# Kernel optimization log

Measured on AMD Instinct MI355X. Metric: run time of the kernel, lower is better.

The kernel has to match this reference:

```python
import jax, jax.numpy as jnp
import numpy as np
import math

H = 16  # heads
EPS = 1e-5

def _gelu_tanh(x):
    c = math.sqrt(2.0 / math.pi)
    return 0.5 * x * (1.0 + jnp.tanh(c * (x + 0.044715 * x * x * x)))

def _layernorm(x, g, b):
    mu = jnp.mean(x, axis=-1, keepdims=True)
    var = jnp.mean((x - mu) ** 2, axis=-1, keepdims=True)
    return (x - mu) / jnp.sqrt(var + EPS) * g + b


def setup_inputs() -> dict:
    key = jax.random.key(0)
    ks = jax.random.split(key, 16)
    B, S, D, F = 8, 1024, 1024, 4096
    s = 1.0 / math.sqrt(D)
    inp = {
        "x": jax.random.normal(ks[0], (B, S, D), jnp.float32),
        "mask": jax.random.randint(ks[1], (B, 1, S, S), 0, 2, jnp.int32),
        "Wq": jax.random.normal(ks[2], (D, D), jnp.float32) * s,
        "bq": jnp.zeros((D,), jnp.float32),
        "Wk": jax.random.normal(ks[3], (D, D), jnp.float32) * s,
        "bk": jnp.zeros((D,), jnp.float32),
        "Wv": jax.random.normal(ks[4], (D, D), jnp.float32) * s,
        "bv": jnp.zeros((D,), jnp.float32),
        "Wo": jax.random.normal(ks[5], (D, D), jnp.float32) * s,
        "bo": jnp.zeros((D,), jnp.float32),
        "W1": jax.random.normal(ks[6], (D, F), jnp.float32) * s,
        "b1": jnp.zeros((F,), jnp.float32),
        "W2": jax.random.normal(ks[7], (F, D), jnp.float32) * (1.0 / math.sqrt(F)),
        "b2": jnp.zeros((D,), jnp.float32),
        "ln1_g": jnp.ones((D,), jnp.float32),
        "ln1_b": jnp.zeros((D,), jnp.float32),
        "ln2_g": jnp.ones((D,), jnp.float32),
        "ln2_b": jnp.zeros((D,), jnp.float32),
    }
    return inp


def reference(x, mask, Wq, bq, Wk, bk, Wv, bv, Wo, bo, W1, b1, W2, b2,
              ln1_g, ln1_b, ln2_g, ln2_b):
    B, S, D = x.shape
    dk = D // H

    # --- sublayer 1: pre-LN multi-head attention + residual ---
    y = _layernorm(x, ln1_g, ln1_b)
    q = (y @ Wq + bq).reshape(B, S, H, dk).transpose(0, 2, 1, 3)  # [B,H,S,dk]
    k = (y @ Wk + bk).reshape(B, S, H, dk).transpose(0, 2, 1, 3)
    v = (y @ Wv + bv).reshape(B, S, H, dk).transpose(0, 2, 1, 3)

    scores = jnp.einsum('bhqd,bhkd->bhqk', q, k) / jnp.sqrt(jnp.float32(dk))
    scores = jnp.where(mask == 0, jnp.float32(-1e9), scores)
    p = jax.nn.softmax(scores, axis=-1)
    a = jnp.einsum('bhqk,bhkd->bhqd', p, v)
    a = a.transpose(0, 2, 1, 3).reshape(B, S, D)
    x = x + (a @ Wo + bo)

    # --- sublayer 2: pre-LN GELU FFN + residual ---
    y = _layernorm(x, ln2_g, ln2_b)
    h = _gelu_tanh(y @ W1 + b1)
    return x + (h @ W2 + b2)
```

## Files before the change

kernel.cpp:

```cpp
#include <hip/hip_runtime.h>
#include <math.h>

typedef unsigned short u16;
typedef short bf16x8 __attribute__((ext_vector_type(8)));
typedef float f32x4 __attribute__((ext_vector_type(4)));

#define DEV static __device__ __forceinline__

DEV float bf2f(u16 u) {
  union { unsigned int i; float f; } v; v.i = ((unsigned int)u) << 16; return v.f;
}
DEV u16 f2bf(float f) {
  union { float f; unsigned int i; } v; v.f = f;
  unsigned int x = v.i;
  return (u16)((x + 0x7FFFu + ((x >> 16) & 1u)) >> 16);
}

DEV void gload16(const void* gsrc, void* ldst) {
  __builtin_amdgcn_global_load_lds(
      (__attribute__((address_space(1))) void*)gsrc,
      (__attribute__((address_space(3))) void*)ldst, 16, 0, 0);
}

DEV f32x4 mfma16(bf16x8 a, bf16x8 b, f32x4 c) {
  return __builtin_amdgcn_mfma_f32_16x16x32_bf16(a, b, c, 0, 0, 0);
}

template <int EPI, int WF32, int NFR>
__global__ __launch_bounds__(512, 2)
void gemm8(const u16* __restrict__ A, const u16* __restrict__ Bt,
           const float* __restrict__ bias, const float* __restrict__ res,
           void* __restrict__ Cv, int M, int N, int K) {
  constexpr int BN = NFR * 64;
  constexpr int HB = NFR * 4096;
  __shared__ __align__(16) char Alds[4 * 16384];
  __shared__ __align__(16) char Blds[4 * HB];

  const int ntn = N / BN;
  const int nwg = gridDim.x;
  const int cpx = nwg >> 3;
  const int bid = (int)blockIdx.x;
  const int swb = (bid & 7) * cpx + (bid >> 3);
  const int tm = swb / ntn, tn = swb % ntn;

  const int tid = threadIdx.x;
  const int wave = tid >> 6, lane = tid & 63;
  const int wm = wave >> 2, wn = wave & 3;
  const int lg = lane >> 4, lr = lane & 15;
  const int swx = (lr & 7) << 4;

  f32x4 acc[8][NFR];
#pragma unroll
  for (int m = 0; m < 8; ++m)
#pragma unroll
    for (int n = 0; n < NFR; ++n)
#pragma unroll
      for (int r = 0; r < 4; ++r) acc[m][n][r] = 0.f;

  const size_t rowb = (size_t)K * 2;
  const char* Ab = (const char*)A + (size_t)tm * 256 * rowb;
  const char* Bb = (const char*)Bt + (size_t)tn * BN * rowb;

  int rowS[2], colS[2];
#pragma unroll
  for (int rr = 0; rr < 2; ++rr) {
    const int p = rr * 8192 + tid * 16;
    const int f = p ^ (((p >> 7) & 7) << 4);
    rowS[rr] = f >> 7; colS[rr] = f & 127;
  }

  const int NT = K >> 6;

#define SA(T, H)                                                              \
  do {                                                                        \
    char* d_ = Alds + ((((T) & 1) * 2 + (H)) << 14);                          \
    _Pragma("unroll")                                                         \
    for (int r_ = 0; r_ < 2; ++r_)                                            \
      gload16(Ab + (size_t)((H) * 128 + rowS[r_]) * rowb + (size_t)(T) * 128  \
                  + colS[r_],                                                 \
              d_ + r_ * 8192 + wave * 1024);                                  \
  } while (0)

#define SB(T, H)                                                              \
  do {                                                                        \
    char* d_ = Blds + ((((T) & 1) * 2 + (H)) * HB);                           \
    _Pragma("unroll")                                                         \
    for (int r_ = 0; r_ < NFR / 2; ++r_)                                      \
      gload16(Bb + (size_t)((H) * (BN / 2) + rowS[r_]) * rowb                 \
                  + (size_t)(T) * 128 + colS[r_],                             \
              d_ + r_ * 8192 + wave * 1024);                                  \
  } while (0)

#define PHASE(SS, Q, STG, DOVM)                                               \
  {                                                                           \
    if ((Q) == 0) {                                                           \
      _Pragma("unroll")                                                       \
      for (int n_ = 0; n_ < NFR; ++n_) {                                      \
        const int g_ = n_ * 4 + wn;                                           \
        const char* bs_ = Blds + ((SS) * 2 + g_ / (NFR * 2)) * HB;            \
        const int rb_ = (g_ % (NFR * 2)) * 16 + lr;                           \
        _Pragma("unroll")                                                     \
        for (int k_ = 0; k_ < 2; ++k_)                                        \
          bfr[n_][k_] =                                                       \
              *(const bf16x8*)(bs_ + ((rb_ * 128 + k_ * 64 + lg * 16) ^ swx));\
      }                                                                       \
    }                                                                         \
    bf16x8 af_[2][2];                                                         \
    {                                                                         \
      const char* as_ = Alds + (((SS) * 2 + ((Q) >> 1)) << 14);               \
      _Pragma("unroll")                                                       \
      for (int j_ = 0; j_ < 2; ++j_) {                                        \
        const int ra_ = ((4 * (Q) + 2 * j_ + wm) & 7) * 16 + lr;              \
        _Pragma("unroll")                                                     \
        for (int k_ = 0; k_ < 2; ++k_)                                        \
          af_[j_][k_] =                                                       \
              *(const bf16x8*)(as_ + ((ra_ * 128 + k_ * 64 + lg * 16) ^ swx));\
      }                                                                       \
    }                                                                         \
    STG;                                                                      \
    if ((Q) == 0) asm volatile("s_waitcnt lgkmcnt(8)");                       \
    if ((DOVM) == 1) {                                                        \
      if (NFR == 4) asm volatile("s_waitcnt vmcnt(6)");                       \
      else          asm volatile("s_waitcnt vmcnt(4)");                       \
    } else if ((DOVM) == 2) {                                                 \
      asm volatile("s_waitcnt vmcnt(0)");                                     \
    }                                                                         \
    __builtin_amdgcn_s_barrier();                                             \
    asm volatile("s_waitcnt lgkmcnt(0)");                                     \
    __builtin_amdgcn_sched_barrier(0);                                        \
    __builtin_amdgcn_s_setprio(1);                                            \
    _Pragma("unroll")                                                         \
    for (int j_ = 0; j_ < 2; ++j_)                                            \
      _Pragma("unroll")                                                       \
      for (int n_ = 0; n_ < NFR; ++n_)                                        \
        _Pragma("unroll")                                                     \
        for (int k_ = 0; k_ < 2; ++k_)                                        \
          acc[2 * (Q) + j_][n_] =                                             \
              mfma16(af_[j_][k_], bfr[n_][k_], acc[2 * (Q) + j_][n_]);        \
    __builtin_amdgcn_s_setprio(0);                                            \
    __builtin_amdgcn_s_barrier();                                             \
  }

  SA(0, 0); SA(0, 1); SB(0, 0); SB(0, 1); SA(1, 0); SB(1, 0); SB(1, 1);
  asm volatile("s_waitcnt vmcnt(0)");
  __builtin_amdgcn_s_barrier();

  bf16x8 bfr[NFR][2];
  const int NIT = NT >> 1;
  for (int it = 0; it < NIT - 1; ++it) {
    const int T0 = 2 * it;
    PHASE(0, 0, SA(T0 + 1, 1), 0)
    PHASE(0, 1, SB(T0 + 2, 0), 0)
    PHASE(0, 2, SA(T0 + 2, 0), 0)
    PHASE(0, 3, SB(T0 + 2, 1), 1)
    PHASE(1, 0, SA(T0 + 2, 1), 0)
    PHASE(1, 1, SB(T0 + 3, 0), 0)
    PHASE(1, 2, SB(T0 + 3, 1), 0)
    PHASE(1, 3, SA(T0 + 3, 0), 1)
  }
  {
    const int T0 = NT - 2;
    PHASE(0, 0, SA(T0 + 1, 1), 0)
    PHASE(0, 1, ((void)0), 0)
    PHASE(0, 2, ((void)0), 0)
    PHASE(0, 3, ((void)0), 2)
    PHASE(1, 0, ((void)0), 0)
    PHASE(1, 1, ((void)0), 0)
    PHASE(1, 2, ((void)0), 0)
    PHASE(1, 3, ((void)0), 0)
  }
#undef SA
#undef SB
#undef PHASE

#pragma unroll
  for (int m = 0; m < 8; ++m)
#pragma unroll
    for (int n = 0; n < NFR; ++n) {
      const int col = tn * BN + (n * 4 + wn) * 16 + lr;
      const float bc = bias[col];
#pragma unroll
      for (int r = 0; r < 4; ++r) {
        const int row = tm * 256 + (2 * m + wm) * 16 + lg * 4 + r;
        float vv = acc[m][n][r] + bc;
        if (EPI == 1) {
          const float u = vv;
          const float z = u + 0.044715f * u * u * u;
          vv = u * __builtin_amdgcn_rcpf(1.0f + exp2f(-2.3022076954f * z));
        } else if (EPI == 2) {
          vv += res[(size_t)row * N + col];
        } else if (EPI == 3) {
          vv *= 0.180336880111112f;
        }
        if (WF32)
          ((float*)Cv)[(size_t)row * N + col] = vv;
        else
          ((u16*)Cv)[(size_t)row * N + col] = f2bf(vv);
      }
    }
}

__global__ __launch_bounds__(256)
void attn_kernel(const u16* __restrict__ Q, const u16* __restrict__ Km,
                 const u16* __restrict__ Vt, const u16* __restrict__ maskT4,
                 u16* __restrict__ O) {
  const int bid = (int)blockIdx.x;
  const int swz = (bid & 7) * 256 + (bid >> 3);
  const int qb = swz & 15;
  const int bh = swz >> 4;
  const int b = bh >> 4, h = bh & 15;
  const int wave = threadIdx.x >> 6, lane = threadIdx.x & 63;
  const int lg = lane >> 4, lr = lane & 15;
  __shared__ __align__(16) u16 Ksm[2][64 * 64];
  __shared__ __align__(16) u16 Vsm[2][64 * 64];
  __shared__ __align__(16) u16 Pl[4][1024];
  char* Pb = (char*)&Pl[wave][0];
  const int swx = (lr & 7) << 4;

  const int q0 = qb * 64 + wave * 16;
  const u16* Qp = Q + ((size_t)(b * 1024 + q0)) * 1024 + h * 64;
  bf16x8 qf[2];
#pragma unroll
  for (int ks = 0; ks < 2; ++ks)
    qf[ks] = *(const bf16x8*)(Qp + (size_t)lr * 1024 + ks * 32 + lg * 8);

  float l = 0.f;
  f32x4 accO[4];
#pragma unroll
  for (int fc = 0; fc < 4; ++fc)
#pragma unroll
    for (int r = 0; r < 4; ++r) accO[fc][r] = 0.f;

  const char* Kg = (const char*)(Km + (size_t)(b * 1024) * 1024 + h * 64);
  const char* Vg = (const char*)(Vt + (size_t)(bh * 64) * 1024);
  const ushort4* Mb0 = (const ushort4*)maskT4 + (size_t)b * 256 * 1024 + q0 + lr;

#define STAGE_KV(T, BUF)                                                      \
  {                                                                           \
    const int kb_ = (T) * 64;                                                 \
    _Pragma("unroll")                                                         \
    for (int c = 0; c < 2; ++c) {                                             \
      const int chunk = wave * 2 + c;                                         \
      const int p = chunk * 1024 + lane * 16;                                 \
      const int f = p ^ (((p >> 7) & 7) << 4);                                \
      const int row = f >> 7, colb = f & 127;                                 \
      gload16(Kg + (size_t)(kb_ + row) * 2048 + colb,                         \
              (char*)Ksm[BUF] + chunk * 1024);                                \
      gload16(Vg + (size_t)row * 2048 + (size_t)kb_ * 2 + colb,               \
              (char*)Vsm[BUF] + chunk * 1024);                                \
    }                                                                         \
  }

  STAGE_KV(0, 0);
  __syncthreads();

  for (int t = 0; t < 16; ++t) {
    const int cb = t & 1;
    if (t < 15) STAGE_KV(t + 1, cb ^ 1);

    ushort4 mv[4];
#pragma unroll
    for (int fc = 0; fc < 4; ++fc)
      mv[fc] = Mb0[(size_t)(t * 16 + fc * 4 + lg) * 1024];

    f32x4 ts[4];
#pragma unroll
    for (int fc = 0; fc < 4; ++fc)
#pragma unroll
      for (int r = 0; r < 4; ++r) ts[fc][r] = 0.f;
    __builtin_amdgcn_s_setprio(1);
#pragma unroll
    for (int ks = 0; ks < 2; ++ks)
#pragma unroll
      for (int fc = 0; fc < 4; ++fc) {
        const int row = fc * 16 + lr;
        const int ad = ((row << 7) | (ks * 64 + lg * 16)) ^ ((row & 7) << 4);
        const bf16x8 kfr = *(const bf16x8*)((const char*)Ksm[cb] + ad);
        ts[fc] = mfma16(kfr, qf[ks], ts[fc]);
      }
    __builtin_amdgcn_s_setprio(0);

#pragma unroll
    for (int fc = 0; fc < 4; ++fc) {
      const float p0 = exp2f(ts[fc][0] + bf2f(mv[fc].x));
      const float p1 = exp2f(ts[fc][1] + bf2f(mv[fc].y));
      const float p2 = exp2f(ts[fc][2] + bf2f(mv[fc].z));
      const float p3 = exp2f(ts[fc][3] + bf2f(mv[fc].w));
      l += (p0 + p1) + (p2 + p3);
      unsigned int w0, w1;
      asm("v_cvt_pk_bf16_f32 %0, %1, %2" : "=v"(w0) : "v"(p0), "v"(p1));
      asm("v_cvt_pk_bf16_f32 %0, %1, %2" : "=v"(w1) : "v"(p2), "v"(p3));
      const int base = lr * 128 + fc * 32 + lg * 8;
      *(unsigned int*)(Pb + ((base + 0) ^ swx)) = w0;
      *(unsigned int*)(Pb + ((base + 4) ^ swx)) = w1;
    }

    __builtin_amdgcn_s_setprio(1);
#pragma unroll
    for (int ks = 0; ks < 2; ++ks) {
      const int ad = (lr * 128 + ks * 64 + lg * 16) ^ swx;
      const bf16x8 pa = *(const bf16x8*)(Pb + ad);
#pragma unroll
      for (int fc = 0; fc < 4; ++fc) {
        const int row = fc * 16 + lr;
        const int vad = ((row << 7) | (ks * 64 + lg * 16)) ^ ((row & 7) << 4);
        const bf16x8 vfr = *(const bf16x8*)((const char*)Vsm[cb] + vad);
        accO[fc] = mfma16(pa, vfr, accO[fc]);
      }
    }
    __builtin_amdgcn_s_setprio(0);

    __syncthreads();
  }

  l += __shfl_xor(l, 16);
  l += __shfl_xor(l, 32);
  float linv[4];
#pragma unroll
  for (int r = 0; r < 4; ++r) linv[r] = 1.0f / __shfl(l, lg * 4 + r);

  u16* Op = O + ((size_t)(b * 1024 + q0)) * 1024 + h * 64;
#pragma unroll
  for (int fc = 0; fc < 4; ++fc)
#pragma unroll
    for (int r = 0; r < 4; ++r)
      Op[(size_t)(lg * 4 + r) * 1024 + fc * 16 + lr] = f2bf(accO[fc][r] * linv[r]);
#undef STAGE_KV
}

__global__ __launch_bounds__(256)
void transpose_cast(const float* __restrict__ in, u16* __restrict__ out, int R, int C) {
  __shared__ u16 t[64][65];
  const int ctiles = C >> 6;
  const int bx = blockIdx.x % ctiles, by = blockIdx.x / ctiles;
  const int tc = threadIdx.x & 63, t4 = threadIdx.x >> 6;
#pragma unroll
  for (int i = 0; i < 16; ++i) {
    const int r = i * 4 + t4;
    t[r][tc] = f2bf(in[(size_t)(by * 64 + r) * C + bx * 64 + tc]);
  }
  __syncthreads();
#pragma unroll
  for (int i = 0; i < 16; ++i) {
    const int r = i * 4 + t4;
    out[(size_t)(bx * 64 + r) * R + by * 64 + tc] = t[tc][r];
  }
}

__global__ __launch_bounds__(256)
void transpose_v_kernel(const u16* __restrict__ v, u16* __restrict__ vt) {
  const int st = blockIdx.x & 15, bh = blockIdx.x >> 4;
  __shared__ u16 t[64][65];
  const int tc = threadIdx.x & 63, t4 = threadIdx.x >> 6;
  const u16* src = v + ((size_t)((bh >> 4) * 1024 + st * 64)) * 1024 + (bh & 15) * 64;
#pragma unroll
  for (int i = 0; i < 16; ++i) {
    const int r = i * 4 + t4;
    t[r][tc] = src[(size_t)r * 1024 + tc];
  }
  __syncthreads();
  u16* dst = vt + (size_t)bh * 64 * 1024 + st * 64;
#pragma unroll
  for (int i = 0; i < 16; ++i) {
    const int r = i * 4 + t4;
    dst[(size_t)r * 1024 + tc] = t[tc][r];
  }
}

__global__ __launch_bounds__(256)
void mask_t_kernel(const int* __restrict__ mask, u16* __restrict__ mt) {
  const int bt = blockIdx.x;
  const int b = bt >> 8;
  const int kt = (bt >> 4) & 15;
  const int qt = bt & 15;
  __shared__ u16 t[64][65];
  const int tc = threadIdx.x & 63, t4 = threadIdx.x >> 6;
  const u16 neg = f2bf(-1.442695040888963e9f);
  const int* src = mask + ((size_t)b * 1024 + qt * 64) * 1024 + kt * 64;
#pragma unroll
  for (int i = 0; i < 16; ++i) {
    const int q = i * 4 + t4;
    t[q][tc] = src[(size_t)q * 1024 + tc] ? (u16)0 : neg;
  }
  __syncthreads();
  ushort4* dst = (ushort4*)mt + ((size_t)b * 256 + kt * 16) * 1024 + qt * 64;
#pragma unroll
  for (int i = 0; i < 4; ++i) {
    const int kg = i * 4 + t4;
    ushort4 o;
    o.x = t[tc][kg * 4 + 0];
    o.y = t[tc][kg * 4 + 1];
    o.z = t[tc][kg * 4 + 2];
    o.w = t[tc][kg * 4 + 3];
    dst[(size_t)kg * 1024 + tc] = o;
  }
}

__global__ __launch_bounds__(256)
void ln_kernel(const float* __restrict__ x, const float* __restrict__ g,
               const float* __restrict__ bb, u16* __restrict__ y) {
  const int row = blockIdx.x, tid = threadIdx.x;
  const float4 v = ((const float4*)(x + (size_t)row * 1024))[tid];
  float s = v.x + v.y + v.z + v.w;
  float ss = v.x * v.x + v.y * v.y + v.z * v.z + v.w * v.w;
#pragma unroll
  for (int mk = 1; mk < 64; mk <<= 1) {
    s += __shfl_xor(s, mk);
    ss += __shfl_xor(ss, mk);
  }
  __shared__ float sa[4], sq[4];
  const int wave = tid >> 6, lane = tid & 63;
  if (lane == 0) { sa[wave] = s; sq[wave] = ss; }
  __syncthreads();
  s = sa[0] + sa[1] + sa[2] + sa[3];
  ss = sq[0] + sq[1] + sq[2] + sq[3];
  const float mu = s * 0.0009765625f;
  const float var = ss * 0.0009765625f - mu * mu;
  const float inv = rsqrtf(var + 1e-5f);
  const float4 gg = ((const float4*)g)[tid];
  const float4 bv = ((const float4*)bb)[tid];
  ushort4 o;
  o.x = f2bf((v.x - mu) * inv * gg.x + bv.x);
  o.y = f2bf((v.y - mu) * inv * gg.y + bv.y);
  o.z = f2bf((v.z - mu) * inv * gg.z + bv.z);
  o.w = f2bf((v.w - mu) * inv * gg.w + bv.w);
  *(ushort4*)(y + (size_t)row * 1024 + tid * 4) = o;
}

extern "C" void kernel_launch(void* const* d_in, const int* in_sizes, int n_in,
                              void* d_out, int out_size, void* d_ws, size_t ws_size,
                              hipStream_t stream) {
  (void)in_sizes; (void)n_in; (void)out_size; (void)ws_size;
  const float* x  = (const float*)d_in[0];
  const int* mask = (const int*)d_in[1];
  const float* Wq = (const float*)d_in[2];  const float* bq = (const float*)d_in[3];
  const float* Wk = (const float*)d_in[4];  const float* bk = (const float*)d_in[5];
  const float* Wv = (const float*)d_in[6];  const float* bv = (const float*)d_in[7];
  const float* Wo = (const float*)d_in[8];  const float* bo = (const float*)d_in[9];
  const float* W1 = (const float*)d_in[10]; const float* b1 = (const float*)d_in[11];
  const float* W2 = (const float*)d_in[12]; const float* b2 = (const float*)d_in[13];
  const float* g1 = (const float*)d_in[14]; const float* be1 = (const float*)d_in[15];
  const float* g2 = (const float*)d_in[16]; const float* be2 = (const float*)d_in[17];

  float* out = (float*)d_out;

  u16* ws = (u16*)d_ws;
  const size_t M1 = (size_t)1024 * 1024;
  u16* y    = ws;
  u16* q    = ws + 8 * M1;
  u16* kbuf = ws + 16 * M1;
  u16* vbuf = ws + 24 * M1;
  u16* vt   = ws + 32 * M1;
  u16* hbuf = ws + 8 * M1;
  u16* wqt  = ws + 40 * M1;
  u16* wkt  = ws + 41 * M1;
  u16* wvt  = ws + 42 * M1;
  u16* wot  = ws + 43 * M1;
  u16* w1t  = ws + 44 * M1;
  u16* w2t  = ws + 48 * M1;
  u16* maskT4 = y;

  dim3 blk(256);
  dim3 blk8(512);
  transpose_cast<<<256, blk, 0, stream>>>(Wq, wqt, 1024, 1024);
  transpose_cast<<<256, blk, 0, stream>>>(Wk, wkt, 1024, 1024);
  transpose_cast<<<256, blk, 0, stream>>>(Wv, wvt, 1024, 1024);
  transpose_cast<<<256, blk, 0, stream>>>(Wo, wot, 1024, 1024);
  transpose_cast<<<1024, blk, 0, stream>>>(W1, w1t, 1024, 4096);
  transpose_cast<<<1024, blk, 0, stream>>>(W2, w2t, 4096, 1024);
  ln_kernel<<<8192, blk, 0, stream>>>(x, g1, be1, y);
  gemm8<3, 0, 2><<<256, blk8, 0, stream>>>(y, wqt, bq, nullptr, q, 8192, 1024, 1024);
  gemm8<0, 0, 2><<<256, blk8, 0, stream>>>(y, wkt, bk, nullptr, kbuf, 8192, 1024, 1024);
  gemm8<0, 0, 2><<<256, blk8, 0, stream>>>(y, wvt, bv, nullptr, vbuf, 8192, 1024, 1024);
  transpose_v_kernel<<<2048, blk, 0, stream>>>(vbuf, vt);
  mask_t_kernel<<<2048, blk, 0, stream>>>(mask, maskT4);
  attn_kernel<<<2048, blk, 0, stream>>>(q, kbuf, vt, maskT4, vbuf);
  gemm8<2, 1, 2><<<256, blk8, 0, stream>>>(vbuf, wot, bo, x, out, 8192, 1024, 1024);
  ln_kernel<<<8192, blk, 0, stream>>>(out, g2, be2, y);
  gemm8<1, 0, 4><<<512, blk8, 0, stream>>>(y, w1t, b1, nullptr, hbuf, 8192, 4096, 1024);
  gemm8<2, 1, 2><<<256, blk8, 0, stream>>>(hbuf, w2t, b2, out, out, 8192, 1024, 4096);
}
```

Before: 404.5 us.

## Double-buffer LDS fragment reads across phases and fix GEMM tile width

```diff
diff --git a/kernel.cpp b/kernel.cpp
--- a/kernel.cpp
+++ b/kernel.cpp
@@ -26,17 +26,15 @@
   return __builtin_amdgcn_mfma_f32_16x16x32_bf16(a, b, c, 0, 0, 0);
 }
 
-template <int EPI, int WF32, int NFR>
+template <int EPI, int WF32>
 __global__ __launch_bounds__(512, 2)
 void gemm8(const u16* __restrict__ A, const u16* __restrict__ Bt,
            const float* __restrict__ bias, const float* __restrict__ res,
            void* __restrict__ Cv, int M, int N, int K) {
-  constexpr int BN = NFR * 64;
-  constexpr int HB = NFR * 4096;
   __shared__ __align__(16) char Alds[4 * 16384];
-  __shared__ __align__(16) char Blds[4 * HB];
-
-  const int ntn = N / BN;
+  __shared__ __align__(16) char Blds[4 * 8192];
+
+  const int ntn = N >> 7;
   const int nwg = gridDim.x;
   const int cpx = nwg >> 3;
   const int bid = (int)blockIdx.x;
@@ -49,17 +47,17 @@
   const int lg = lane >> 4, lr = lane & 15;
   const int swx = (lr & 7) << 4;
 
-  f32x4 acc[8][NFR];
+  f32x4 acc[8][2];
 #pragma unroll
   for (int m = 0; m < 8; ++m)
 #pragma unroll
-    for (int n = 0; n < NFR; ++n)
+    for (int n = 0; n < 2; ++n)
 #pragma unroll
       for (int r = 0; r < 4; ++r) acc[m][n][r] = 0.f;
 
   const size_t rowb = (size_t)K * 2;
   const char* Ab = (const char*)A + (size_t)tm * 256 * rowb;
-  const char* Bb = (const char*)Bt + (size_t)tn * BN * rowb;
+  const char* Bb = (const char*)Bt + (size_t)tn * 128 * rowb;
 
   int rowS[2], colS[2];
 #pragma unroll
@@ -83,101 +81,112 @@
 
 #define SB(T, H)                                                              \
   do {                                                                        \
-    char* d_ = Blds + ((((T) & 1) * 2 + (H)) * HB);                           \
-    _Pragma("unroll")                                                         \
-    for (int r_ = 0; r_ < NFR / 2; ++r_)                                      \
-      gload16(Bb + (size_t)((H) * (BN / 2) + rowS[r_]) * rowb                 \
-                  + (size_t)(T) * 128 + colS[r_],                             \
-              d_ + r_ * 8192 + wave * 1024);                                  \
+    char* d_ = Blds + ((((T) & 1) * 2 + (H)) * 8192);                         \
+    gload16(Bb + (size_t)((H) * 64 + rowS[0]) * rowb + (size_t)(T) * 128      \
+                + colS[0],                                                    \
+            d_ + wave * 1024);                                                \
   } while (0)
 
-#define PHASE(SS, Q, STG, DOVM)                                               \
+#define RDA(BUF, NSS, NQ)                                                     \
   {                                                                           \
-    if ((Q) == 0) {                                                           \
+    const char* as_ = Alds + (((NSS) * 2 + ((NQ) >> 1)) << 14);               \
+    _Pragma("unroll")                                                         \
+    for (int j_ = 0; j_ < 2; ++j_) {                                          \
+      const int ra_ = ((4 * (NQ) + 2 * j_ + wm) & 7) * 16 + lr;               \
       _Pragma("unroll")                                                       \
-      for (int n_ = 0; n_ < NFR; ++n_) {                                      \
-        const int g_ = n_ * 4 + wn;                                           \
-        const char* bs_ = Blds + ((SS) * 2 + g_ / (NFR * 2)) * HB;            \
-        const int rb_ = (g_ % (NFR * 2)) * 16 + lr;                           \
-        _Pragma("unroll")                                                     \
-        for (int k_ = 0; k_ < 2; ++k_)                                        \
-          bfr[n_][k_] =                                                       \
-              *(const bf16x8*)(bs_ + ((rb_ * 128 + k_ * 64 + lg * 16) ^ swx));\
-      }                                                                       \
+      for (int k_ = 0; k_ < 2; ++k_)                                          \
+        afr[BUF][j_][k_] =                                                    \
+            *(const bf16x8*)(as_ + ((ra_ * 128 + k_ * 64 + lg * 16) ^ swx));  \
     }                                                                         \
-    bf16x8 af_[2][2];                                                         \
-    {                                                                         \
-      const char* as_ = Alds + (((SS) * 2 + ((Q) >> 1)) << 14);               \
+  }
+
+#define RDB(BUF, NSS)                                                         \
+  {                                                                           \
+    _Pragma("unroll")                                                         \
+    for (int n_ = 0; n_ < 2; ++n_) {                                          \
+      const char* bs_ = Blds + ((NSS) * 2 + n_) * 8192;                       \
+      const int rb_ = wn * 16 + lr;                                           \
       _Pragma("unroll")                                                       \
-      for (int j_ = 0; j_ < 2; ++j_) {                                        \
-        const int ra_ = ((4 * (Q) + 2 * j_ + wm) & 7) * 16 + lr;              \
-        _Pragma("unroll")                                                     \
-        for (int k_ = 0; k_ < 2; ++k_)                                        \
-          af_[j_][k_] =                                                       \
-              *(const bf16x8*)(as_ + ((ra_ * 128 + k_ * 64 + lg * 16) ^ swx));\
-      }                                                                       \
+      for (int k_ = 0; k_ < 2; ++k_)                                          \
+        bfr[BUF][n_][k_] =                                                    \
+            *(const bf16x8*)(bs_ + ((rb_ * 128 + k_ * 64 + lg * 16) ^ swx));  \
     }                                                                         \
+  }
+
+#define PHASE(CUR, BB, Q, STG, DOVM, DON, NSS, NQ, DOB)                       \
+  {                                                                           \
     STG;                                                                      \
-    if ((Q) == 0) asm volatile("s_waitcnt lgkmcnt(8)");                       \
-    if ((DOVM) == 1) {                                                        \
-      if (NFR == 4) asm volatile("s_waitcnt vmcnt(6)");                       \
-      else          asm volatile("s_waitcnt vmcnt(4)");                       \
-    } else if ((DOVM) == 2) {                                                 \
-      asm volatile("s_waitcnt vmcnt(0)");                                     \
-    }                                                                         \
+    if ((DOVM) == 1) asm volatile("s_waitcnt vmcnt(4)");                      \
+    else if ((DOVM) == 2) asm volatile("s_waitcnt vmcnt(0)");                 \
     __builtin_amdgcn_s_barrier();                                             \
     asm volatile("s_waitcnt lgkmcnt(0)");                                     \
     __builtin_amdgcn_sched_barrier(0);                                        \
     __builtin_amdgcn_s_setprio(1);                                            \
     _Pragma("unroll")                                                         \
-    for (int j_ = 0; j_ < 2; ++j_)                                            \
+    for (int n_ = 0; n_ < 2; ++n_)                                            \
       _Pragma("unroll")                                                       \
-      for (int n_ = 0; n_ < NFR; ++n_)                                        \
-        _Pragma("unroll")                                                     \
-        for (int k_ = 0; k_ < 2; ++k_)                                        \
-          acc[2 * (Q) + j_][n_] =                                             \
-              mfma16(af_[j_][k_], bfr[n_][k_], acc[2 * (Q) + j_][n_]);        \
+      for (int k_ = 0; k_ < 2; ++k_)                                          \
+        acc[2 * (Q) + 0][n_] =                                                \
+            mfma16(afr[CUR][0][k_], bfr[BB][n_][k_], acc[2 * (Q) + 0][n_]);   \
+    __builtin_amdgcn_sched_barrier(0);                                        \
+    if (DON) {                                                                \
+      RDA((CUR) ^ 1, NSS, NQ);                                                \
+      if (DOB) RDB((BB) ^ 1, NSS);                                            \
+    }                                                                         \
+    __builtin_amdgcn_sched_barrier(0);                                        \
+    _Pragma("unroll")                                                         \
+    for (int n_ = 0; n_ < 2; ++n_)                                            \
+      _Pragma("unroll")                                                       \
+      for (int k_ = 0; k_ < 2; ++k_)                                          \
+        acc[2 * (Q) + 1][n_] =                                                \
+            mfma16(afr[CUR][1][k_], bfr[BB][n_][k_], acc[2 * (Q) + 1][n_]);   \
     __builtin_amdgcn_s_setprio(0);                                            \
     __builtin_amdgcn_s_barrier();                                             \
   }
+
+  bf16x8 afr[2][2][2];
+  bf16x8 bfr[2][2][2];
 
   SA(0, 0); SA(0, 1); SB(0, 0); SB(0, 1); SA(1, 0); SB(1, 0); SB(1, 1);
   asm volatile("s_waitcnt vmcnt(0)");
   __builtin_amdgcn_s_barrier();
-
-  bf16x8 bfr[NFR][2];
+  RDA(0, 0, 0);
+  RDB(0, 0);
+
   const int NIT = NT >> 1;
   for (int it = 0; it < NIT - 1; ++it) {
     const int T0 = 2 * it;
-    PHASE(0, 0, SA(T0 + 1, 1), 0)
-    PHASE(0, 1, SB(T0 + 2, 0), 0)
-    PHASE(0, 2, SA(T0 + 2, 0), 0)
-    PHASE(0, 3, SB(T0 + 2, 1), 1)
-    PHASE(1, 0, SA(T0 + 2, 1), 0)
-    PHASE(1, 1, SB(T0 + 3, 0), 0)
-    PHASE(1, 2, SB(T0 + 3, 1), 0)
-    PHASE(1, 3, SA(T0 + 3, 0), 1)
+    PHASE(0, 0, 0, SA(T0 + 1, 1), 0, 1, 0, 1, 0)
+    PHASE(1, 0, 1, SB(T0 + 2, 0), 0, 1, 0, 2, 0)
+    PHASE(0, 0, 2, SA(T0 + 2, 0), 0, 1, 0, 3, 0)
+    PHASE(1, 0, 3, SB(T0 + 2, 1), 1, 1, 1, 0, 1)
+    PHASE(0, 1, 0, SA(T0 + 2, 1), 0, 1, 1, 1, 0)
+    PHASE(1, 1, 1, SB(T0 + 3, 0), 0, 1, 1, 2, 0)
+    PHASE(0, 1, 2, SB(T0 + 3, 1), 0, 1, 1, 3, 0)
+    PHASE(1, 1, 3, SA(T0 + 3, 0), 1, 1, 0, 0, 1)
   }
   {
     const int T0 = NT - 2;
-    PHASE(0, 0, SA(T0 + 1, 1), 0)
-    PHASE(0, 1, ((void)0), 0)
-    PHASE(0, 2, ((void)0), 0)
-    PHASE(0, 3, ((void)0), 2)
-    PHASE(1, 0, ((void)0), 0)
-    PHASE(1, 1, ((void)0), 0)
-    PHASE(1, 2, ((void)0), 0)
-    PHASE(1, 3, ((void)0), 0)
+    PHASE(0, 0, 0, SA(T0 + 1, 1), 0, 1, 0, 1, 0)
+    PHASE(1, 0, 1, ((void)0), 0, 1, 0, 2, 0)
+    PHASE(0, 0, 2, ((void)0), 0, 1, 0, 3, 0)
+    PHASE(1, 0, 3, ((void)0), 2, 1, 1, 0, 1)
+    PHASE(0, 1, 0, ((void)0), 0, 1, 1, 1, 0)
+    PHASE(1, 1, 1, ((void)0), 0, 1, 1, 2, 0)
+    PHASE(0, 1, 2, ((void)0), 0, 1, 1, 3, 0)
+    PHASE(1, 1, 3, ((void)0), 0, 0, 0, 0, 0)
   }
 #undef SA
 #undef SB
+#undef RDA
+#undef RDB
 #undef PHASE
 
 #pragma unroll
   for (int m = 0; m < 8; ++m)
 #pragma unroll
-    for (int n = 0; n < NFR; ++n) {
-      const int col = tn * BN + (n * 4 + wn) * 16 + lr;
+    for (int n = 0; n < 2; ++n) {
+      const int col = tn * 128 + (n * 4 + wn) * 16 + lr;
       const float bc = bias[col];
 #pragma unroll
       for (int r = 0; r < 4; ++r) {
@@ -469,14 +478,14 @@
   transpose_cast<<<1024, blk, 0, stream>>>(W1, w1t, 1024, 4096);
   transpose_cast<<<1024, blk, 0, stream>>>(W2, w2t, 4096, 1024);
   ln_kernel<<<8192, blk, 0, stream>>>(x, g1, be1, y);
-  gemm8<3, 0, 2><<<256, blk8, 0, stream>>>(y, wqt, bq, nullptr, q, 8192, 1024, 1024);
-  gemm8<0, 0, 2><<<256, blk8, 0, stream>>>(y, wkt, bk, nullptr, kbuf, 8192, 1024, 1024);
-  gemm8<0, 0, 2><<<256, blk8, 0, stream>>>(y, wvt, bv, nullptr, vbuf, 8192, 1024, 1024);
+  gemm8<3, 0><<<256, blk8, 0, stream>>>(y, wqt, bq, nullptr, q, 8192, 1024, 1024);
+  gemm8<0, 0><<<256, blk8, 0, stream>>>(y, wkt, bk, nullptr, kbuf, 8192, 1024, 1024);
+  gemm8<0, 0><<<256, blk8, 0, stream>>>(y, wvt, bv, nullptr, vbuf, 8192, 1024, 1024);
   transpose_v_kernel<<<2048, blk, 0, stream>>>(vbuf, vt);
   mask_t_kernel<<<2048, blk, 0, stream>>>(mask, maskT4);
   attn_kernel<<<2048, blk, 0, stream>>>(q, kbuf, vt, maskT4, vbuf);
-  gemm8<2, 1, 2><<<256, blk8, 0, stream>>>(vbuf, wot, bo, x, out, 8192, 1024, 1024);
+  gemm8<2, 1><<<256, blk8, 0, stream>>>(vbuf, wot, bo, x, out, 8192, 1024, 1024);
   ln_kernel<<<8192, blk, 0, stream>>>(out, g2, be2, y);
-  gemm8<1, 0, 4><<<512, blk8, 0, stream>>>(y, w1t, b1, nullptr, hbuf, 8192, 4096, 1024);
-  gemm8<2, 1, 2><<<256, blk8, 0, stream>>>(hbuf, w2t, b2, out, out, 8192, 1024, 4096);
-}
+  gemm8<1, 0><<<1024, blk8, 0, stream>>>(y, w1t, b1, nullptr, hbuf, 8192, 4096, 1024);
+  gemm8<2, 1><<<256, blk8, 0, stream>>>(hbuf, w2t, b2, out, out, 8192, 1024, 4096);
+}
```

Measured after the change: 433.1 us. +7.1%, slower.

## Split GEMM phases into 4x(NFR/2) quadrants and reschedule B-tile prefetch

Applied to the files above, without the earlier changes.

```diff
diff --git a/kernel.cpp b/kernel.cpp
--- a/kernel.cpp
+++ b/kernel.cpp
@@ -33,6 +33,7 @@
            void* __restrict__ Cv, int M, int N, int K) {
   constexpr int BN = NFR * 64;
   constexpr int HB = NFR * 4096;
+  constexpr int NH = NFR / 2;
   __shared__ __align__(16) char Alds[4 * 16384];
   __shared__ __align__(16) char Blds[4 * HB];
 
@@ -85,7 +86,7 @@
   do {                                                                        \
     char* d_ = Blds + ((((T) & 1) * 2 + (H)) * HB);                           \
     _Pragma("unroll")                                                         \
-    for (int r_ = 0; r_ < NFR / 2; ++r_)                                      \
+    for (int r_ = 0; r_ < NH; ++r_)                                           \
       gload16(Bb + (size_t)((H) * (BN / 2) + rowS[r_]) * rowb                 \
                   + (size_t)(T) * 128 + colS[r_],                             \
               d_ + r_ * 8192 + wave * 1024);                                  \
@@ -93,74 +94,75 @@
 
 #define PHASE(SS, Q, STG, DOVM)                                               \
   {                                                                           \
-    if ((Q) == 0) {                                                           \
-      _Pragma("unroll")                                                       \
-      for (int n_ = 0; n_ < NFR; ++n_) {                                      \
-        const int g_ = n_ * 4 + wn;                                           \
-        const char* bs_ = Blds + ((SS) * 2 + g_ / (NFR * 2)) * HB;            \
-        const int rb_ = (g_ % (NFR * 2)) * 16 + lr;                           \
-        _Pragma("unroll")                                                     \
-        for (int k_ = 0; k_ < 2; ++k_)                                        \
-          bfr[n_][k_] =                                                       \
-              *(const bf16x8*)(bs_ + ((rb_ * 128 + k_ * 64 + lg * 16) ^ swx));\
-      }                                                                       \
-    }                                                                         \
-    bf16x8 af_[2][2];                                                         \
+    bf16x8 af_[4][2], bf_[NH][2];                                             \
     {                                                                         \
       const char* as_ = Alds + (((SS) * 2 + ((Q) >> 1)) << 14);               \
       _Pragma("unroll")                                                       \
-      for (int j_ = 0; j_ < 2; ++j_) {                                        \
-        const int ra_ = ((4 * (Q) + 2 * j_ + wm) & 7) * 16 + lr;              \
+      for (int j_ = 0; j_ < 4; ++j_) {                                        \
+        const int ra_ = (2 * j_ + wm) * 16 + lr;                              \
         _Pragma("unroll")                                                     \
         for (int k_ = 0; k_ < 2; ++k_)                                        \
           af_[j_][k_] =                                                       \
               *(const bf16x8*)(as_ + ((ra_ * 128 + k_ * 64 + lg * 16) ^ swx));\
       }                                                                       \
+      const char* bs_ = Blds + ((SS) * 2 + ((Q) & 1)) * HB;                   \
+      _Pragma("unroll")                                                       \
+      for (int n_ = 0; n_ < NH; ++n_) {                                       \
+        const int rb_ = (n_ * 4 + wn) * 16 + lr;                              \
+        _Pragma("unroll")                                                     \
+        for (int k_ = 0; k_ < 2; ++k_)                                        \
+          bf_[n_][k_] =                                                       \
+              *(const bf16x8*)(bs_ + ((rb_ * 128 + k_ * 64 + lg * 16) ^ swx));\
+      }                                                                       \
     }                                                                         \
     STG;                                                                      \
-    if ((Q) == 0) asm volatile("s_waitcnt lgkmcnt(8)");                       \
+    __builtin_amdgcn_sched_barrier(0);                                        \
     if ((DOVM) == 1) {                                                        \
-      if (NFR == 4) asm volatile("s_waitcnt vmcnt(6)");                       \
-      else          asm volatile("s_waitcnt vmcnt(4)");                       \
+      if (NFR == 4) asm volatile("s_waitcnt vmcnt(4)" ::: "memory");          \
+      else          asm volatile("s_waitcnt vmcnt(3)" ::: "memory");          \
     } else if ((DOVM) == 2) {                                                 \
-      asm volatile("s_waitcnt vmcnt(0)");                                     \
+      asm volatile("s_waitcnt vmcnt(0)" ::: "memory");                        \
     }                                                                         \
     __builtin_amdgcn_s_barrier();                                             \
-    asm volatile("s_waitcnt lgkmcnt(0)");                                     \
+    asm volatile("s_waitcnt lgkmcnt(0)" ::: "memory");                        \
     __builtin_amdgcn_sched_barrier(0);                                        \
     __builtin_amdgcn_s_setprio(1);                                            \
     _Pragma("unroll")                                                         \
-    for (int j_ = 0; j_ < 2; ++j_)                                            \
+    for (int j_ = 0; j_ < 4; ++j_)                                            \
       _Pragma("unroll")                                                       \
-      for (int n_ = 0; n_ < NFR; ++n_)                                        \
+      for (int n_ = 0; n_ < NH; ++n_)                                         \
         _Pragma("unroll")                                                     \
         for (int k_ = 0; k_ < 2; ++k_)                                        \
-          acc[2 * (Q) + j_][n_] =                                             \
-              mfma16(af_[j_][k_], bfr[n_][k_], acc[2 * (Q) + j_][n_]);        \
+          acc[4 * ((Q) >> 1) + j_][((Q) & 1) * NH + n_] =                     \
+              mfma16(af_[j_][k_], bf_[n_][k_],                                \
+                     acc[4 * ((Q) >> 1) + j_][((Q) & 1) * NH + n_]);          \
     __builtin_amdgcn_s_setprio(0);                                            \
+    __builtin_amdgcn_sched_barrier(0);                                        \
     __builtin_amdgcn_s_barrier();                                             \
-  }
-
-  SA(0, 0); SA(0, 1); SB(0, 0); SB(0, 1); SA(1, 0); SB(1, 0); SB(1, 1);
-  asm volatile("s_waitcnt vmcnt(0)");
+    __builtin_amdgcn_sched_barrier(0);                                        \
+  }
+
+  SA(0, 0); SA(0, 1); SB(0, 0); SB(0, 1); SA(1, 0); SB(1, 0);
+  __builtin_amdgcn_sched_barrier(0);
+  asm volatile("s_waitcnt vmcnt(0)" ::: "memory");
   __builtin_amdgcn_s_barrier();
-
-  bf16x8 bfr[NFR][2];
+  __builtin_amdgcn_sched_barrier(0);
+
   const int NIT = NT >> 1;
   for (int it = 0; it < NIT - 1; ++it) {
     const int T0 = 2 * it;
-    PHASE(0, 0, SA(T0 + 1, 1), 0)
-    PHASE(0, 1, SB(T0 + 2, 0), 0)
+    PHASE(0, 0, { SA(T0 + 1, 1); SB(T0 + 1, 1); }, 0)
+    PHASE(0, 1, ((void)0), 0)
     PHASE(0, 2, SA(T0 + 2, 0), 0)
-    PHASE(0, 3, SB(T0 + 2, 1), 1)
+    PHASE(0, 3, SB(T0 + 2, 0), 1)
     PHASE(1, 0, SA(T0 + 2, 1), 0)
-    PHASE(1, 1, SB(T0 + 3, 0), 0)
-    PHASE(1, 2, SB(T0 + 3, 1), 0)
-    PHASE(1, 3, SA(T0 + 3, 0), 1)
+    PHASE(1, 1, SB(T0 + 2, 1), 0)
+    PHASE(1, 2, SA(T0 + 3, 0), 0)
+    PHASE(1, 3, SB(T0 + 3, 0), 1)
   }
   {
     const int T0 = NT - 2;
-    PHASE(0, 0, SA(T0 + 1, 1), 0)
+    PHASE(0, 0, { SA(T0 + 1, 1); SB(T0 + 1, 1); }, 0)
     PHASE(0, 1, ((void)0), 0)
     PHASE(0, 2, ((void)0), 0)
     PHASE(0, 3, ((void)0), 2)
```

New measurement: 436.9 us. 1.08x slower.
